# Kernel optimization log

Hardware: AMD Instinct MI355X
Metric: run time of the kernel (lower is better)

The kernel has to match this reference:

```python
import jax, jax.numpy as jnp
import numpy as np

VOCAB = 50000
EMB = 256
HID = 256
MAX_PRED = 30
B = 64
S_ENC = 100


def setup_inputs() -> dict:
    key = jax.random.key(0)
    ks = jax.random.split(key, 16)
    s = 1.0 / np.sqrt(HID)
    return {
        "comment": jax.random.randint(ks[0], (B, 29), 0, VOCAB),
        "comment_input": jax.random.randint(ks[1], (B, 30), 0, VOCAB),
        "tok_output": jax.random.normal(ks[2], (B, S_ENC, HID), jnp.float32),
        "tok_enc_hc": jax.random.normal(ks[3], (1, B, HID), jnp.float32),
        "sbtao_output": jax.random.normal(ks[4], (B, S_ENC, HID), jnp.float32),
        "wemb": jax.random.normal(ks[5], (VOCAB, EMB), jnp.float32) * 0.02,
        "W_ih": jax.random.uniform(ks[6], (3 * HID, EMB), jnp.float32, -s, s),
        "W_hh": jax.random.uniform(ks[7], (3 * HID, HID), jnp.float32, -s, s),
        "b_ih": jax.random.uniform(ks[8], (3 * HID,), jnp.float32, -s, s),
        "b_hh": jax.random.uniform(ks[9], (3 * HID,), jnp.float32, -s, s),
        "W1": jax.random.uniform(ks[10], (HID, 3 * HID), jnp.float32, -s, s),
        "b1": jax.random.uniform(ks[11], (HID,), jnp.float32, -s, s),
        "W2": jax.random.uniform(ks[12], (VOCAB, HID), jnp.float32, -s, s),
        "b2": jax.random.uniform(ks[13], (VOCAB,), jnp.float32, -s, s),
    }


def _decode(comment_input, T, tok_output, h0, sbtao_output,
            wemb, W_ih, W_hh, b_ih, b_hh, W1, b1, W2, b2):
    # h0: [B,H]. The torch code re-uses hidden=tok_enc_hc at EVERY step,
    # so each step is an independent GRU-cell step -> vectorize over T.
    bsz = comment_input.shape[0]
    H = h0.shape[-1]
    emb = wemb[comment_input[:, :T]]                      # [B,T,E]
    gi = emb @ W_ih.T + b_ih                              # [B,T,3H]
    gh = h0 @ W_hh.T + b_hh                               # [B,3H]
    gh = gh[:, None, :]                                   # broadcast over T
    r = jax.nn.sigmoid(gi[..., :H] + gh[..., :H])
    z = jax.nn.sigmoid(gi[..., H:2 * H] + gh[..., H:2 * H])
    n = jnp.tanh(gi[..., 2 * H:] + r * gh[..., 2 * H:])
    dec = (1.0 - z) * n + z * h0[:, None, :]              # [B,T,H]

    def attend(enc):  # enc: [B,S,H]
        S = enc.shape[1]
        # Faithful to torch: keys come from a RESHAPE [B,S,H] -> [B,H,S]
        # (memory reinterpretation), not a transpose.
        keys = enc.reshape(bsz, H, S)
        a = jax.nn.softmax(jnp.einsum('bth,bhs->bts', dec, keys), axis=-1)
        return jnp.einsum('bts,bsh->bth', a, enc)         # [B,T,H]

    ctx = attend(tok_output)
    ast_ctx = attend(sbtao_output)
    cat = jnp.concatenate([ctx, dec, ast_ctx], axis=-1)   # [B,T,3H]
    out = jax.nn.relu(cat @ W1.T + b1)                    # [B,T,H]
    out = jax.nn.relu(out @ W2.T + b2)                    # [B,T,V]
    logprobs = jax.nn.log_softmax(out, axis=-1)           # [B,T,V]
    return logprobs


def reference(comment, comment_input, tok_output, tok_enc_hc, sbtao_output,
              wemb, W_ih, W_hh, b_ih, b_hh, W1, b1, W2, b2):
    T = min(comment.shape[1] + 1, MAX_PRED)
    h0 = tok_enc_hc[0]
    logprobs = _decode(comment_input, T, tok_output, h0, sbtao_output,
                       wemb, W_ih, W_hh, b_ih, b_hh, W1, b1, W2, b2)
    seq = jnp.argmax(logprobs, axis=-1).astype(jnp.int64 if jax.config.jax_enable_x64 else jnp.int32)
    return seq, logprobs
```

## Files before the change

kernel.cpp:

```cpp
#include <hip/hip_runtime.h>
#include <hip/hip_bf16.h>
#include <math.h>

#define NROW 1920
#define VOCAB_ 50000
#define NPAD 50048
#define NBLK 391
#define CAP 128

typedef __attribute__((ext_vector_type(8))) short short8;
typedef __attribute__((ext_vector_type(4))) float floatx4;

__device__ inline ushort f32_to_bf16_bits(float f) {
    union { float f; unsigned u; } v; v.f = f;
    unsigned u = v.u;
    u += 0x7fffu + ((u >> 16) & 1u);
    return (ushort)(u >> 16);
}

__global__ void gather_emb_kernel(const int* __restrict__ tokens,
                                  const float* __restrict__ wemb,
                                  float* __restrict__ emb) {
    int n = blockIdx.x;
    int e = threadIdx.x;
    int tok = tokens[n];
    emb[(size_t)n * 256 + e] = wemb[(size_t)tok * 256 + e];
}

template <bool RELU>
__global__ __launch_bounds__(256) void gemm_nt_kernel(
    const float* __restrict__ A, const float* __restrict__ Bm,
    const float* __restrict__ bias, float* __restrict__ C,
    ushort* __restrict__ Cbf,
    int M, int N, int K) {
    __shared__ float As[32][68];
    __shared__ float Bs[32][68];

    const int tid = threadIdx.x;
    const int m0 = blockIdx.y * 64;
    const int n0 = blockIdx.x * 64;
    const int tx = tid & 15;
    const int ty = tid >> 4;
    const int lrow = tid >> 3;
    const int lcol = (tid & 7) * 4;

    float acc[4][4];
#pragma unroll
    for (int i = 0; i < 4; ++i)
#pragma unroll
        for (int j = 0; j < 4; ++j) acc[i][j] = 0.f;

    for (int k0 = 0; k0 < K; k0 += 32) {
#pragma unroll
        for (int half = 0; half < 2; ++half) {
            int m = lrow + half * 32;
            float4 av = *reinterpret_cast<const float4*>(
                A + (size_t)(m0 + m) * K + k0 + lcol);
            As[lcol + 0][m] = av.x; As[lcol + 1][m] = av.y;
            As[lcol + 2][m] = av.z; As[lcol + 3][m] = av.w;
            int n = lrow + half * 32;
            float4 bv = make_float4(0.f, 0.f, 0.f, 0.f);
            if (n0 + n < N)
                bv = *reinterpret_cast<const float4*>(
                    Bm + (size_t)(n0 + n) * K + k0 + lcol);
            Bs[lcol + 0][n] = bv.x; Bs[lcol + 1][n] = bv.y;
            Bs[lcol + 2][n] = bv.z; Bs[lcol + 3][n] = bv.w;
        }
        __syncthreads();
#pragma unroll
        for (int k = 0; k < 32; ++k) {
            float4 a4 = *reinterpret_cast<const float4*>(&As[k][ty * 4]);
            float4 b4 = *reinterpret_cast<const float4*>(&Bs[k][tx * 4]);
            float a[4] = {a4.x, a4.y, a4.z, a4.w};
            float b[4] = {b4.x, b4.y, b4.z, b4.w};
#pragma unroll
            for (int i = 0; i < 4; ++i)
#pragma unroll
                for (int j = 0; j < 4; ++j) acc[i][j] = fmaf(a[i], b[j], acc[i][j]);
        }
        __syncthreads();
    }
#pragma unroll
    for (int i = 0; i < 4; ++i) {
        int m = m0 + ty * 4 + i;
#pragma unroll
        for (int j = 0; j < 4; ++j) {
            int n = n0 + tx * 4 + j;
            if (n < N) {
                float v = acc[i][j] + bias[n];
                if (RELU) v = fmaxf(v, 0.f);
                C[(size_t)m * N + n] = v;
                if (Cbf) Cbf[(size_t)m * N + n] = f32_to_bf16_bits(v);
            }
        }
    }
}

__global__ void dec_kernel(const float* __restrict__ gi,
                           const float* __restrict__ gh,
                           const float* __restrict__ h0,
                           float* __restrict__ cat) {
    int n = blockIdx.x;
    int h = threadIdx.x;
    int b = n / 30;
    float gir = gi[(size_t)n * 768 + h];
    float giz = gi[(size_t)n * 768 + 256 + h];
    float gin = gi[(size_t)n * 768 + 512 + h];
    float ghr = gh[(size_t)b * 768 + h];
    float ghz = gh[(size_t)b * 768 + 256 + h];
    float ghn = gh[(size_t)b * 768 + 512 + h];
    float r = 1.f / (1.f + expf(-(gir + ghr)));
    float z = 1.f / (1.f + expf(-(giz + ghz)));
    float nn = tanhf(gin + r * ghn);
    float h0v = h0[(size_t)b * 256 + h];
    cat[(size_t)n * 768 + 256 + h] = (1.f - z) * nn + z * h0v;
}

__global__ __launch_bounds__(256) void attn_kernel(
    const float* __restrict__ enc, float* __restrict__ cat, int colbase) {
    __shared__ float decs[256];
    __shared__ float sc[100];
    __shared__ float red[2];

    int n = blockIdx.x;
    int b = n / 30;
    int tid = threadIdx.x;

    decs[tid] = cat[(size_t)n * 768 + 256 + tid];
    __syncthreads();
    const float* e = enc + (size_t)b * 25600;
    if (tid < 100) {
        float acc = 0.f;
        for (int h = 0; h < 256; ++h) acc = fmaf(decs[h], e[h * 100 + tid], acc);
        sc[tid] = acc;
    }
    __syncthreads();
    if (tid == 0) {
        float mx = sc[0];
        for (int s = 1; s < 100; ++s) mx = fmaxf(mx, sc[s]);
        red[0] = mx;
    }
    __syncthreads();
    if (tid < 100) sc[tid] = expf(sc[tid] - red[0]);
    __syncthreads();
    if (tid == 0) {
        float sum = 0.f;
        for (int s = 0; s < 100; ++s) sum += sc[s];
        red[1] = 1.f / sum;
    }
    __syncthreads();
    float inv = red[1];
    float acc = 0.f;
    for (int s = 0; s < 100; ++s) acc = fmaf(sc[s], e[s * 256 + tid], acc);
    cat[(size_t)n * 768 + colbase + tid] = acc * inv;
}

__global__ void conv_w2_kernel(const float* __restrict__ W2, ushort* __restrict__ Wb) {
    int row = blockIdx.x;
    int col = threadIdx.x;
    float v = (row < VOCAB_) ? W2[(size_t)row * 256 + col] : 0.f;
    Wb[(size_t)row * 256 + col] = f32_to_bf16_bits(v);
}

template <int MODE>
__global__ __launch_bounds__(256) void mfma_gemm_kernel(
    const ushort* __restrict__ Abf, const ushort* __restrict__ Bbf,
    const float* __restrict__ b2, float* __restrict__ C,
    float* __restrict__ pmax, float* __restrict__ psum,
    const float* __restrict__ row_max, const float* __restrict__ row_lse,
    int* __restrict__ cnt, int* __restrict__ cand) {
    __shared__ ushort As[128 * 64];
    __shared__ ushort Bs[128 * 64];
    __shared__ float pmL[128][2];
    __shared__ float psL[128][2];

    const int tid = threadIdx.x;
    const int m0 = blockIdx.x * 128;
    const int n0 = blockIdx.y * 128;
    const int nblk = blockIdx.y;
    const int wave = tid >> 6, lane = tid & 63;
    const int wm = wave >> 1, wn = wave & 1;
    const int q = lane >> 4, ln = lane & 15;

    const int lrow = lane >> 3;
    const int lcol8 = (lane & 7) * 8;

    floatx4 acc[4][4];
#pragma unroll
    for (int i = 0; i < 4; ++i)
#pragma unroll
        for (int j = 0; j < 4; ++j) acc[i][j] = (floatx4)0.f;

    for (int k0 = 0; k0 < 256; k0 += 64) {
        __syncthreads();
#pragma unroll
        for (int c = 0; c < 4; ++c) {
            int rbase = wave * 32 + c * 8;
            const ushort* ga = Abf + (size_t)(m0 + rbase + lrow) * 256 + k0 + lcol8;
            const ushort* gb = Bbf + (size_t)(n0 + rbase + lrow) * 256 + k0 + lcol8;
            __builtin_amdgcn_global_load_lds(
                (const __attribute__((address_space(1))) unsigned int*)ga,
                (__attribute__((address_space(3))) unsigned int*)&As[rbase * 64],
                16, 0, 0);
            __builtin_amdgcn_global_load_lds(
                (const __attribute__((address_space(1))) unsigned int*)gb,
                (__attribute__((address_space(3))) unsigned int*)&Bs[rbase * 64],
                16, 0, 0);
        }
        __syncthreads();
#pragma unroll
        for (int ks = 0; ks < 2; ++ks) {
            short8 af[4], bf[4];
#pragma unroll
            for (int mt = 0; mt < 4; ++mt)
                af[mt] = *reinterpret_cast<const short8*>(
                    &As[(wm * 64 + mt * 16 + ln) * 64 + ks * 32 + q * 8]);
#pragma unroll
            for (int nt = 0; nt < 4; ++nt)
                bf[nt] = *reinterpret_cast<const short8*>(
                    &Bs[(wn * 64 + nt * 16 + ln) * 64 + ks * 32 + q * 8]);
#pragma unroll
            for (int mt = 0; mt < 4; ++mt)
#pragma unroll
                for (int nt = 0; nt < 4; ++nt)
                    acc[mt][nt] = __builtin_amdgcn_mfma_f32_16x16x32_bf16(
                        af[mt], bf[nt], acc[mt][nt], 0, 0, 0);
        }
    }

    float bias[4]; int nn[4];
#pragma unroll
    for (int nt = 0; nt < 4; ++nt) {
        int n = n0 + wn * 64 + nt * 16 + ln;
        nn[nt] = n;
        bias[nt] = (n < VOCAB_) ? b2[n] : 0.f;
    }

    if (MODE == 0) {
#pragma unroll
        for (int mt = 0; mt < 4; ++mt) {
#pragma unroll
            for (int r = 0; r < 4; ++r) {
                float vv[4]; float lmax = -1e30f;
#pragma unroll
                for (int nt = 0; nt < 4; ++nt) {
                    float v = acc[mt][nt][r] + bias[nt];
                    v = fmaxf(v, 0.f);
                    if (nn[nt] >= VOCAB_) v = -1e30f;
                    vv[nt] = v;
                    lmax = fmaxf(lmax, v);
                }
#pragma unroll
                for (int off = 1; off < 16; off <<= 1)
                    lmax = fmaxf(lmax, __shfl_xor(lmax, off, 64));
                float ls = 0.f;
#pragma unroll
                for (int nt = 0; nt < 4; ++nt) ls += __expf(vv[nt] - lmax);
#pragma unroll
                for (int off = 1; off < 16; off <<= 1)
                    ls += __shfl_xor(ls, off, 64);
                if (ln == 0) {
                    int rl = wm * 64 + mt * 16 + q * 4 + r;
                    pmL[rl][wn] = lmax;
                    psL[rl][wn] = ls;
                }
            }
        }
        __syncthreads();
        if (tid < 128) {
            float m1 = pmL[tid][0], m2 = pmL[tid][1];
            float nm = fmaxf(m1, m2);
            float s = psL[tid][0] * __expf(m1 - nm) + psL[tid][1] * __expf(m2 - nm);
            pmax[(size_t)(m0 + tid) * NBLK + nblk] = nm;
            psum[(size_t)(m0 + tid) * NBLK + nblk] = s;
        }
    } else {
#pragma unroll
        for (int mt = 0; mt < 4; ++mt) {
#pragma unroll
            for (int r = 0; r < 4; ++r) {
                int m = m0 + wm * 64 + mt * 16 + q * 4 + r;
                float thr = row_max[m] - 0.03f;
                float rl = row_lse[m];
#pragma unroll
                for (int nt = 0; nt < 4; ++nt) {
                    if (nn[nt] < VOCAB_) {
                        float v = acc[mt][nt][r] + bias[nt];
                        v = fmaxf(v, 0.f);
                        C[(size_t)m * VOCAB_ + nn[nt]] = v - rl;
                        if (v >= thr) {
                            int k = atomicAdd(&cnt[m], 1);
                            if (k < CAP) cand[m * CAP + k] = nn[nt];
                        }
                    }
                }
            }
        }
    }
}

__global__ __launch_bounds__(128) void reduce_rows_kernel(
    const float* __restrict__ pmax, const float* __restrict__ psum,
    float* __restrict__ row_max, float* __restrict__ row_lse,
    int* __restrict__ cnt) {
    __shared__ float sm[128], ss[128];
    int row = blockIdx.x, tid = threadIdx.x;
    if (tid == 0) cnt[row] = 0;
    const float* pm = pmax + (size_t)row * NBLK;
    const float* ps = psum + (size_t)row * NBLK;
    float m = -1e30f, s = 0.f;
    for (int i = tid; i < NBLK; i += 128) {
        float m2 = pm[i], s2 = ps[i];
        float nm = fmaxf(m, m2);
        s = s * __expf(m - nm) + s2 * __expf(m2 - nm);
        m = nm;
    }
    sm[tid] = m; ss[tid] = s;
    __syncthreads();
    for (int off = 64; off > 0; off >>= 1) {
        if (tid < off) {
            float m2 = sm[tid + off], s2 = ss[tid + off];
            float nm = fmaxf(sm[tid], m2);
            ss[tid] = ss[tid] * __expf(sm[tid] - nm) + s2 * __expf(m2 - nm);
            sm[tid] = nm;
        }
        __syncthreads();
    }
    if (tid == 0) {
        row_max[row] = sm[0];
        row_lse[row] = sm[0] + logf(ss[0]);
    }
}

__global__ __launch_bounds__(256) void final_cand_kernel(
    const int* __restrict__ cnt, const int* __restrict__ cand,
    const float* __restrict__ out1, const float* __restrict__ W2,
    const float* __restrict__ b2, float* __restrict__ seq) {
    __shared__ float o1s[256];
    __shared__ double red[256];
    __shared__ double bestv_s;
    __shared__ int besti_s;

    int row = blockIdx.x, tid = threadIdx.x;
    if (tid == 0) { bestv_s = -1e300; besti_s = 0x7fffffff; }
    o1s[tid] = out1[(size_t)row * 256 + tid];
    __syncthreads();

    int nc = min(cnt[row], CAP);
    for (int j = 0; j < nc; ++j) {
        int c = cand[row * CAP + j];
        red[tid] = (double)o1s[tid] * (double)W2[(size_t)c * 256 + tid];
        __syncthreads();
        for (int off = 128; off > 0; off >>= 1) {
            if (tid < off) red[tid] += red[tid + off];
            __syncthreads();
        }
        if (tid == 0) {
            double v = red[0] + (double)b2[c];
            if (v < 0.0) v = 0.0;
            if (v > bestv_s || (v == bestv_s && c < besti_s)) { bestv_s = v; besti_s = c; }
        }
        __syncthreads();
    }
    if (tid == 0) seq[row] = (float)(besti_s == 0x7fffffff ? 0 : besti_s);
}

extern "C" void kernel_launch(void* const* d_in, const int* in_sizes, int n_in,
                              void* d_out, int out_size, void* d_ws, size_t ws_size,
                              hipStream_t stream) {
    const int* comment_input = (const int*)d_in[1];
    const float* tok_output  = (const float*)d_in[2];
    const float* h0          = (const float*)d_in[3];
    const float* sbtao       = (const float*)d_in[4];
    const float* wemb        = (const float*)d_in[5];
    const float* W_ih        = (const float*)d_in[6];
    const float* W_hh        = (const float*)d_in[7];
    const float* b_ih        = (const float*)d_in[8];
    const float* b_hh        = (const float*)d_in[9];
    const float* W1          = (const float*)d_in[10];
    const float* b1          = (const float*)d_in[11];
    const float* W2          = (const float*)d_in[12];
    const float* b2          = (const float*)d_in[13];

    float* out    = (float*)d_out;
    float* seq    = out;
    float* logits = out + NROW;

    float* ws      = (float*)d_ws;
    float* emb     = ws;
    float* gi      = emb + 491520;
    float* gh      = gi + 1474560;
    float* cat     = gh + 49152;
    float* out1    = cat + 1474560;
    float* pmax    = out1 + 491520;
    float* psum    = pmax + 750720;
    float* row_max = psum + 750720;
    float* row_lse = row_max + 1920;
    ushort* out1b  = (ushort*)(row_lse + 1920);
    ushort* W2b    = (ushort*)(row_lse + 1920 + 245760);
    int* cnt       = (int*)emb;
    int* cand      = cnt + 1920;

    gather_emb_kernel<<<NROW, 256, 0, stream>>>(comment_input, wemb, emb);

    gemm_nt_kernel<false><<<dim3(12, 1), 256, 0, stream>>>(
        h0, W_hh, b_hh, gh, nullptr, 64, 768, 256);
    gemm_nt_kernel<false><<<dim3(12, 30), 256, 0, stream>>>(
        emb, W_ih, b_ih, gi, nullptr, NROW, 768, 256);
    dec_kernel<<<NROW, 256, 0, stream>>>(gi, gh, h0, cat);
    attn_kernel<<<NROW, 256, 0, stream>>>(tok_output, cat, 0);
    attn_kernel<<<NROW, 256, 0, stream>>>(sbtao, cat, 512);
    gemm_nt_kernel<true><<<dim3(4, 30), 256, 0, stream>>>(
        cat, W1, b1, out1, out1b, NROW, 256, 768);

    conv_w2_kernel<<<NPAD, 256, 0, stream>>>(W2, W2b);

    mfma_gemm_kernel<0><<<dim3(15, NBLK), 256, 0, stream>>>(
        out1b, W2b, b2, logits, pmax, psum, nullptr, nullptr, nullptr, nullptr);

    reduce_rows_kernel<<<NROW, 128, 0, stream>>>(pmax, psum, row_max, row_lse, cnt);

    mfma_gemm_kernel<1><<<dim3(15, NBLK), 256, 0, stream>>>(
        out1b, W2b, b2, logits, nullptr, nullptr, row_max, row_lse, cnt, cand);

    final_cand_kernel<<<NROW, 256, 0, stream>>>(
        cnt, cand, out1, W2, b2, seq);
}
```

Measured before the change: 873.9 us.

## Fuse embedding gather into front GEMMs and merge GRU cell with both attentions

The embedding gather now happens inside the GEMM that computes the input gates, reading wemb rows by token index directly, and the W_hh GEMM runs in the same launch as extra blocks. The GRU cell and both attention passes are combined into one per-row kernel that keeps the decoder state in shared memory. The serial single-thread max and sum in attention are replaced with tree reductions. This removes several launches and the emb and dec round trips through global memory, at the cost of more barriers per block.

Result: faster. 845.6 us (-3.2%).

```diff
diff --git a/kernel.cpp b/kernel.cpp
--- a/kernel.cpp
+++ b/kernel.cpp
@@ -18,13 +18,153 @@
     return (ushort)(u >> 16);
 }
 
-__global__ void gather_emb_kernel(const int* __restrict__ tokens,
-                                  const float* __restrict__ wemb,
-                                  float* __restrict__ emb) {
+__global__ __launch_bounds__(256) void front_gemm_kernel(
+    const float* __restrict__ h0, const float* __restrict__ W_hh,
+    const float* __restrict__ b_hh, float* __restrict__ gh,
+    const int* __restrict__ tokens, const float* __restrict__ wemb,
+    const float* __restrict__ W_ih, const float* __restrict__ b_ih,
+    float* __restrict__ gi) {
+    __shared__ float As[32][68];
+    __shared__ float Bs[32][68];
+    __shared__ int tok_s[64];
+
+    const int tid = threadIdx.x;
+    const int bid = blockIdx.x;
+    const bool is_gh = (bid < 12);
+
+    int m0, n0;
+    const float* Bm;
+    const float* bias;
+    float* C;
+    if (is_gh) {
+        m0 = 0; n0 = bid * 64; Bm = W_hh; bias = b_hh; C = gh;
+    } else {
+        int bb = bid - 12;
+        m0 = (bb / 12) * 64; n0 = (bb % 12) * 64;
+        Bm = W_ih; bias = b_ih; C = gi;
+    }
+
+    if (!is_gh && tid < 64) tok_s[tid] = tokens[m0 + tid];
+    __syncthreads();
+
+    const int tx = tid & 15;
+    const int ty = tid >> 4;
+    const int lrow = tid >> 3;
+    const int lcol = (tid & 7) * 4;
+
+    float acc[4][4];
+#pragma unroll
+    for (int i = 0; i < 4; ++i)
+#pragma unroll
+        for (int j = 0; j < 4; ++j) acc[i][j] = 0.f;
+
+    for (int k0 = 0; k0 < 256; k0 += 32) {
+#pragma unroll
+        for (int half = 0; half < 2; ++half) {
+            int m = lrow + half * 32;
+            const float* arow = is_gh ? (h0 + (size_t)(m0 + m) * 256)
+                                      : (wemb + (size_t)tok_s[m] * 256);
+            float4 av = *reinterpret_cast<const float4*>(arow + k0 + lcol);
+            As[lcol + 0][m] = av.x; As[lcol + 1][m] = av.y;
+            As[lcol + 2][m] = av.z; As[lcol + 3][m] = av.w;
+            int n = lrow + half * 32;
+            float4 bv = *reinterpret_cast<const float4*>(
+                Bm + (size_t)(n0 + n) * 256 + k0 + lcol);
+            Bs[lcol + 0][n] = bv.x; Bs[lcol + 1][n] = bv.y;
+            Bs[lcol + 2][n] = bv.z; Bs[lcol + 3][n] = bv.w;
+        }
+        __syncthreads();
+#pragma unroll
+        for (int k = 0; k < 32; ++k) {
+            float4 a4 = *reinterpret_cast<const float4*>(&As[k][ty * 4]);
+            float4 b4 = *reinterpret_cast<const float4*>(&Bs[k][tx * 4]);
+            float a[4] = {a4.x, a4.y, a4.z, a4.w};
+            float b[4] = {b4.x, b4.y, b4.z, b4.w};
+#pragma unroll
+            for (int i = 0; i < 4; ++i)
+#pragma unroll
+                for (int j = 0; j < 4; ++j) acc[i][j] = fmaf(a[i], b[j], acc[i][j]);
+        }
+        __syncthreads();
+    }
+#pragma unroll
+    for (int i = 0; i < 4; ++i) {
+        int m = m0 + ty * 4 + i;
+#pragma unroll
+        for (int j = 0; j < 4; ++j) {
+            int n = n0 + tx * 4 + j;
+            C[(size_t)m * 768 + n] = acc[i][j] + bias[n];
+        }
+    }
+}
+
+__global__ void conv_w2_kernel(const float* __restrict__ W2, ushort* __restrict__ Wb) {
+    int row = blockIdx.x;
+    int col = threadIdx.x;
+    float v = (row < VOCAB_) ? W2[(size_t)row * 256 + col] : 0.f;
+    Wb[(size_t)row * 256 + col] = f32_to_bf16_bits(v);
+}
+
+__global__ __launch_bounds__(256) void dec_attn_kernel(
+    const float* __restrict__ gi, const float* __restrict__ gh,
+    const float* __restrict__ h0, const float* __restrict__ tok_output,
+    const float* __restrict__ sbtao, float* __restrict__ cat) {
+    __shared__ float decs[256];
+    __shared__ float sc[100];
+    __shared__ float redbuf[128];
+
     int n = blockIdx.x;
-    int e = threadIdx.x;
-    int tok = tokens[n];
-    emb[(size_t)n * 256 + e] = wemb[(size_t)tok * 256 + e];
+    int b = n / 30;
+    int tid = threadIdx.x;
+
+    float gir = gi[(size_t)n * 768 + tid];
+    float giz = gi[(size_t)n * 768 + 256 + tid];
+    float gin = gi[(size_t)n * 768 + 512 + tid];
+    float ghr = gh[(size_t)b * 768 + tid];
+    float ghz = gh[(size_t)b * 768 + 256 + tid];
+    float ghn = gh[(size_t)b * 768 + 512 + tid];
+    float r = 1.f / (1.f + expf(-(gir + ghr)));
+    float z = 1.f / (1.f + expf(-(giz + ghz)));
+    float nnv = tanhf(gin + r * ghn);
+    float d = (1.f - z) * nnv + z * h0[(size_t)b * 256 + tid];
+    decs[tid] = d;
+    cat[(size_t)n * 768 + 256 + tid] = d;
+    __syncthreads();
+
+    for (int a = 0; a < 2; ++a) {
+        const float* e = (a == 0 ? tok_output : sbtao) + (size_t)b * 25600;
+        int colbase = (a == 0) ? 0 : 512;
+        if (tid < 100) {
+            float acc = 0.f;
+            for (int h = 0; h < 256; ++h)
+                acc = fmaf(decs[h], e[h * 100 + tid], acc);
+            sc[tid] = acc;
+        }
+        __syncthreads();
+        if (tid < 128) redbuf[tid] = (tid < 100) ? sc[tid] : -1e30f;
+        __syncthreads();
+        for (int off = 64; off > 0; off >>= 1) {
+            if (tid < off) redbuf[tid] = fmaxf(redbuf[tid], redbuf[tid + off]);
+            __syncthreads();
+        }
+        float mx = redbuf[0];
+        __syncthreads();
+        if (tid < 100) sc[tid] = expf(sc[tid] - mx);
+        __syncthreads();
+        if (tid < 128) redbuf[tid] = (tid < 100) ? sc[tid] : 0.f;
+        __syncthreads();
+        for (int off = 64; off > 0; off >>= 1) {
+            if (tid < off) redbuf[tid] += redbuf[tid + off];
+            __syncthreads();
+        }
+        float inv = 1.f / redbuf[0];
+        __syncthreads();
+        float acc = 0.f;
+        for (int s = 0; s < 100; ++s)
+            acc = fmaf(sc[s], e[(size_t)s * 256 + tid], acc);
+        cat[(size_t)n * 768 + colbase + tid] = acc * inv;
+        __syncthreads();
+    }
 }
 
 template <bool RELU>
@@ -94,72 +234,6 @@
             }
         }
     }
-}
-
-__global__ void dec_kernel(const float* __restrict__ gi,
-                           const float* __restrict__ gh,
-                           const float* __restrict__ h0,
-                           float* __restrict__ cat) {
-    int n = blockIdx.x;
-    int h = threadIdx.x;
-    int b = n / 30;
-    float gir = gi[(size_t)n * 768 + h];
-    float giz = gi[(size_t)n * 768 + 256 + h];
-    float gin = gi[(size_t)n * 768 + 512 + h];
-    float ghr = gh[(size_t)b * 768 + h];
-    float ghz = gh[(size_t)b * 768 + 256 + h];
-    float ghn = gh[(size_t)b * 768 + 512 + h];
-    float r = 1.f / (1.f + expf(-(gir + ghr)));
-    float z = 1.f / (1.f + expf(-(giz + ghz)));
-    float nn = tanhf(gin + r * ghn);
-    float h0v = h0[(size_t)b * 256 + h];
-    cat[(size_t)n * 768 + 256 + h] = (1.f - z) * nn + z * h0v;
-}
-
-__global__ __launch_bounds__(256) void attn_kernel(
-    const float* __restrict__ enc, float* __restrict__ cat, int colbase) {
-    __shared__ float decs[256];
-    __shared__ float sc[100];
-    __shared__ float red[2];
-
-    int n = blockIdx.x;
-    int b = n / 30;
-    int tid = threadIdx.x;
-
-    decs[tid] = cat[(size_t)n * 768 + 256 + tid];
-    __syncthreads();
-    const float* e = enc + (size_t)b * 25600;
-    if (tid < 100) {
-        float acc = 0.f;
-        for (int h = 0; h < 256; ++h) acc = fmaf(decs[h], e[h * 100 + tid], acc);
-        sc[tid] = acc;
-    }
-    __syncthreads();
-    if (tid == 0) {
-        float mx = sc[0];
-        for (int s = 1; s < 100; ++s) mx = fmaxf(mx, sc[s]);
-        red[0] = mx;
-    }
-    __syncthreads();
-    if (tid < 100) sc[tid] = expf(sc[tid] - red[0]);
-    __syncthreads();
-    if (tid == 0) {
-        float sum = 0.f;
-        for (int s = 0; s < 100; ++s) sum += sc[s];
-        red[1] = 1.f / sum;
-    }
-    __syncthreads();
-    float inv = red[1];
-    float acc = 0.f;
-    for (int s = 0; s < 100; ++s) acc = fmaf(sc[s], e[s * 256 + tid], acc);
-    cat[(size_t)n * 768 + colbase + tid] = acc * inv;
-}
-
-__global__ void conv_w2_kernel(const float* __restrict__ W2, ushort* __restrict__ Wb) {
-    int row = blockIdx.x;
-    int col = threadIdx.x;
-    float v = (row < VOCAB_) ? W2[(size_t)row * 256 + col] : 0.f;
-    Wb[(size_t)row * 256 + col] = f32_to_bf16_bits(v);
 }
 
 template <int MODE>
@@ -387,8 +461,8 @@
     float* logits = out + NROW;
 
     float* ws      = (float*)d_ws;
-    float* emb     = ws;
-    float* gi      = emb + 491520;
+    float* scratch = ws;
+    float* gi      = scratch + 491520;
     float* gh      = gi + 1474560;
     float* cat     = gh + 49152;
     float* out1    = cat + 1474560;
@@ -398,23 +472,20 @@
     float* row_lse = row_max + 1920;
     ushort* out1b  = (ushort*)(row_lse + 1920);
     ushort* W2b    = (ushort*)(row_lse + 1920 + 245760);
-    int* cnt       = (int*)emb;
+    int* cnt       = (int*)scratch;
     int* cand      = cnt + 1920;
 
-    gather_emb_kernel<<<NROW, 256, 0, stream>>>(comment_input, wemb, emb);
-
-    gemm_nt_kernel<false><<<dim3(12, 1), 256, 0, stream>>>(
-        h0, W_hh, b_hh, gh, nullptr, 64, 768, 256);
-    gemm_nt_kernel<false><<<dim3(12, 30), 256, 0, stream>>>(
-        emb, W_ih, b_ih, gi, nullptr, NROW, 768, 256);
-    dec_kernel<<<NROW, 256, 0, stream>>>(gi, gh, h0, cat);
-    attn_kernel<<<NROW, 256, 0, stream>>>(tok_output, cat, 0);
-    attn_kernel<<<NROW, 256, 0, stream>>>(sbtao, cat, 512);
+    front_gemm_kernel<<<372, 256, 0, stream>>>(
+        h0, W_hh, b_hh, gh, comment_input, wemb, W_ih, b_ih, gi);
+
+    conv_w2_kernel<<<NPAD, 256, 0, stream>>>(W2, W2b);
+
+    dec_attn_kernel<<<NROW, 256, 0, stream>>>(
+        gi, gh, h0, tok_output, sbtao, cat);
+
     gemm_nt_kernel<true><<<dim3(4, 30), 256, 0, stream>>>(
         cat, W1, b1, out1, out1b, NROW, 256, 768);
 
-    conv_w2_kernel<<<NPAD, 256, 0, stream>>>(W2, W2b);
-
     mfma_gemm_kernel<0><<<dim3(15, NBLK), 256, 0, stream>>>(
         out1b, W2b, b2, logits, pmax, psum, nullptr, nullptr, nullptr, nullptr);
 
```
